# Performance work log

Measured on AMD Instinct MI355X. Metric: run time of the kernel, lower is better.

## Reference

```python
import jax, jax.numpy as jnp
import numpy as np

N_NODES = 50000
N_EDGES = 800000


def _spmm(edge_row, edge_col, edge_w, h):
    # sparse adj @ h via gather + segment-sum: adj[r,c] = edge_w
    msgs = edge_w[:, None] * h[edge_col]          # [E, D] gather
    return jax.ops.segment_sum(msgs, edge_row, num_segments=N_NODES)


def setup_inputs() -> dict:
    key = jax.random.key(0)
    ks = jax.random.split(key, 8)
    x = jax.random.normal(ks[0], (N_NODES, 256), dtype=jnp.float32)
    edge_row = jax.random.randint(ks[1], (N_EDGES,), 0, N_NODES, dtype=jnp.int32)
    edge_col = jax.random.randint(ks[2], (N_EDGES,), 0, N_NODES, dtype=jnp.int32)
    edge_w = jax.random.uniform(ks[3], (N_EDGES,), dtype=jnp.float32)
    W1 = jax.random.normal(ks[4], (256, 128), dtype=jnp.float32) * 0.06
    b1 = jnp.zeros((128,), dtype=jnp.float32)
    W2 = jax.random.normal(ks[5], (128, 32), dtype=jnp.float32) * 0.09
    b2 = jnp.zeros((32,), dtype=jnp.float32)
    return {"x": x, "edge_row": edge_row, "edge_col": edge_col,
            "edge_w": edge_w, "W1": W1, "b1": b1, "W2": W2, "b2": b2}


def reference(x, edge_row, edge_col, edge_w, W1, b1, W2, b2):
    # Layer 1: support = X @ W1 ; out = relu(A @ support + b1)
    # (dropout is identity in eval mode)
    h = jax.nn.relu(_spmm(edge_row, edge_col, edge_w, x @ W1) + b1)
    # Layer 2
    out = jax.nn.relu(_spmm(edge_row, edge_col, edge_w, h @ W2) + b2)
    return out
```

## Files before the change

### kernel.cpp

```cpp
#include <hip/hip_runtime.h>

#define N_NODES 50000
#define N_EDGES 800000
#define D0 256
#define D1 128
#define D2 32
#define CAP 64
#define SCAT_BLOCKS 391
#define G1_BLOCKS 782

typedef unsigned short u16;
typedef unsigned int   u32;
typedef __attribute__((ext_vector_type(8))) short bf16x8;
typedef __attribute__((ext_vector_type(4))) float f32x4;

__device__ inline u32 bf16rne(float f) {
    union { float f; u32 u; } c; c.f = f;
    return (c.u + 0x7FFFu + ((c.u >> 16) & 1u)) >> 16;
}
__device__ inline float bfhi(u32 v) {
    union { u32 u; float f; } c; c.u = v & 0xFFFF0000u; return c.f;
}
__device__ inline float bflo(u32 v) {
    union { u32 u; float f; } c; c.u = v << 16; return c.f;
}

__global__ __launch_bounds__(256) void front_kernel(const float* __restrict__ W1,
                                                    u16* __restrict__ Bsw1,
                                                    const float* __restrict__ W2,
                                                    u16* __restrict__ Bsw2) {
    const int bid = blockIdx.x;
    if (bid < 16) {
        const int id = bid * 256 + threadIdx.x;
        const int lane = id & 63;
        const int t    = (id >> 6) & 7;
        const int ks   = id >> 9;
        const int n     = t * 16 + (lane & 15);
        const int kbase = ks * 32 + (lane >> 4) * 8;
        u32 v[8];
        #pragma unroll
        for (int j = 0; j < 8; ++j) v[j] = bf16rne(W1[(kbase + j) * D1 + n]);
        uint4 w;
        w.x = v[0] | (v[1] << 16);
        w.y = v[2] | (v[3] << 16);
        w.z = v[4] | (v[5] << 16);
        w.w = v[6] | (v[7] << 16);
        ((uint4*)Bsw1)[id] = w;
    } else {
        const int id = (bid - 16) * 256 + threadIdx.x;
        const int lane = id & 63;
        const int t    = (id >> 6) & 1;
        const int ks   = id >> 7;
        const int n     = t * 16 + (lane & 15);
        const int kbase = ks * 32 + (lane >> 4) * 8;
        u32 v[8];
        #pragma unroll
        for (int j = 0; j < 8; ++j) v[j] = bf16rne(W2[(kbase + j) * D2 + n]);
        uint4 w;
        w.x = v[0] | (v[1] << 16);
        w.y = v[2] | (v[3] << 16);
        w.z = v[4] | (v[5] << 16);
        w.w = v[6] | (v[7] << 16);
        ((uint4*)Bsw2)[id] = w;
    }
}

__global__ __launch_bounds__(256) void mid_kernel(const float* __restrict__ x,
                                                  const u16* __restrict__ Bsw1,
                                                  u16* __restrict__ s1b,
                                                  const int* __restrict__ erow,
                                                  const int* __restrict__ ecol,
                                                  const float* __restrict__ ew,
                                                  int* __restrict__ cnt,
                                                  u32* __restrict__ eg) {
    const int bid = blockIdx.x;
    if (bid < G1_BLOCKS) {
        const int lane = threadIdx.x & 63;
        const int wave = threadIdx.x >> 6;
        const int rowbase = bid * 64 + wave * 16;
        const int m    = lane & 15;
        const int quad = lane >> 4;
        int arow = rowbase + m;
        if (arow >= N_NODES) arow = N_NODES - 1;
        const float* aptr = x + (size_t)arow * D0 + quad * 8;

        f32x4 acc[8];
        #pragma unroll
        for (int t = 0; t < 8; ++t) acc[t] = (f32x4){0.f, 0.f, 0.f, 0.f};

        #pragma unroll
        for (int ks = 0; ks < 8; ++ks) {
            const float4 f0 = *(const float4*)(aptr + ks * 32);
            const float4 f1 = *(const float4*)(aptr + ks * 32 + 4);
            bf16x8 a;
            a[0] = (short)bf16rne(f0.x); a[1] = (short)bf16rne(f0.y);
            a[2] = (short)bf16rne(f0.z); a[3] = (short)bf16rne(f0.w);
            a[4] = (short)bf16rne(f1.x); a[5] = (short)bf16rne(f1.y);
            a[6] = (short)bf16rne(f1.z); a[7] = (short)bf16rne(f1.w);
            const u16* bp = Bsw1 + ((size_t)(ks * 8) * 64 + lane) * 8;
            #pragma unroll
            for (int t = 0; t < 8; ++t) {
                const bf16x8 b = *(const bf16x8*)(bp + (size_t)t * 64 * 8);
                acc[t] = __builtin_amdgcn_mfma_f32_16x16x32_bf16(a, b, acc[t], 0, 0, 0);
            }
        }
        const int orow = rowbase + quad * 4;
        #pragma unroll
        for (int r = 0; r < 4; ++r) {
            const int row = orow + r;
            if (row < N_NODES) {
                u16* op = s1b + (size_t)row * D1 + m;
                #pragma unroll
                for (int t = 0; t < 8; ++t) op[t * 16] = (u16)bf16rne(acc[t][r]);
            }
        }
    } else {
        const int base = (bid - G1_BLOCKS) * 2048 + threadIdx.x;
        int  rows[8], cols[8];
        float ws[8];
        bool valid[8];
        #pragma unroll
        for (int k = 0; k < 8; ++k) {
            const int e = base + k * 256;
            valid[k] = e < N_EDGES;
            if (valid[k]) { rows[k] = erow[e]; cols[k] = ecol[e]; ws[k] = ew[e]; }
        }
        #pragma unroll
        for (int k = 0; k < 8; ++k) {
            if (valid[k]) {
                const int p = atomicAdd(&cnt[rows[k]], 1);
                if (p < CAP)
                    eg[(size_t)rows[k] * CAP + p] = (u32)cols[k] | (bf16rne(ws[k]) << 16);
            }
        }
    }
}

__global__ __launch_bounds__(256) void spmm_csr128_kernel(const int* __restrict__ cnt,
                                                          const u32* __restrict__ eg,
                                                          const u16* __restrict__ src,
                                                          const float* __restrict__ bias,
                                                          u16* __restrict__ dst) {
    const int lane = threadIdx.x;
    const int row  = blockIdx.x * 8 + threadIdx.y;
    if (row >= N_NODES) return;
    int len = cnt[row];
    if (len > CAP) len = CAP;
    const u32* ep = eg + (size_t)row * CAP;
    float4 a0 = {0.f,0.f,0.f,0.f}, a1 = {0.f,0.f,0.f,0.f};
    float4 a2 = {0.f,0.f,0.f,0.f}, a3 = {0.f,0.f,0.f,0.f};
    int j = 0;
    for (; j + 3 < len; j += 4) {
        const uint4 e4 = *(const uint4*)(ep + j);
        const uint2 v0 = ((const uint2*)(src + (size_t)(e4.x & 0xFFFFu) * D1))[lane];
        const uint2 v1 = ((const uint2*)(src + (size_t)(e4.y & 0xFFFFu) * D1))[lane];
        const uint2 v2 = ((const uint2*)(src + (size_t)(e4.z & 0xFFFFu) * D1))[lane];
        const uint2 v3 = ((const uint2*)(src + (size_t)(e4.w & 0xFFFFu) * D1))[lane];
        const float w0 = bfhi(e4.x), w1 = bfhi(e4.y), w2 = bfhi(e4.z), w3 = bfhi(e4.w);
        a0.x += w0 * bflo(v0.x); a0.y += w0 * bfhi(v0.x);
        a0.z += w0 * bflo(v0.y); a0.w += w0 * bfhi(v0.y);
        a1.x += w1 * bflo(v1.x); a1.y += w1 * bfhi(v1.x);
        a1.z += w1 * bflo(v1.y); a1.w += w1 * bfhi(v1.y);
        a2.x += w2 * bflo(v2.x); a2.y += w2 * bfhi(v2.x);
        a2.z += w2 * bflo(v2.y); a2.w += w2 * bfhi(v2.y);
        a3.x += w3 * bflo(v3.x); a3.y += w3 * bfhi(v3.x);
        a3.z += w3 * bflo(v3.y); a3.w += w3 * bfhi(v3.y);
    }
    for (; j < len; ++j) {
        const u32 e0 = ep[j];
        const float w0 = bfhi(e0);
        const uint2 v0 = ((const uint2*)(src + (size_t)(e0 & 0xFFFFu) * D1))[lane];
        a0.x += w0 * bflo(v0.x); a0.y += w0 * bfhi(v0.x);
        a0.z += w0 * bflo(v0.y); a0.w += w0 * bfhi(v0.y);
    }
    const float4 b4 = ((const float4*)bias)[lane];
    float rx = a0.x + a1.x + a2.x + a3.x + b4.x; rx = rx > 0.f ? rx : 0.f;
    float ry = a0.y + a1.y + a2.y + a3.y + b4.y; ry = ry > 0.f ? ry : 0.f;
    float rz = a0.z + a1.z + a2.z + a3.z + b4.z; rz = rz > 0.f ? rz : 0.f;
    float rw = a0.w + a1.w + a2.w + a3.w + b4.w; rw = rw > 0.f ? rw : 0.f;
    uint2 o;
    o.x = bf16rne(rx) | (bf16rne(ry) << 16);
    o.y = bf16rne(rz) | (bf16rne(rw) << 16);
    ((uint2*)(dst + (size_t)row * D1))[lane] = o;
}

__global__ __launch_bounds__(256) void gemm2_mfma_kernel(const u16* __restrict__ hb,
                                                         const u16* __restrict__ Bsw2,
                                                         u16* __restrict__ s2b) {
    const int lane = threadIdx.x & 63;
    const int wave = threadIdx.x >> 6;
    const int rowbase = blockIdx.x * 64 + wave * 16;
    const int m    = lane & 15;
    const int quad = lane >> 4;
    int arow = rowbase + m;
    if (arow >= N_NODES) arow = N_NODES - 1;
    const u16* aptr = hb + (size_t)arow * D1 + quad * 8;

    f32x4 acc0 = (f32x4){0.f,0.f,0.f,0.f};
    f32x4 acc1 = (f32x4){0.f,0.f,0.f,0.f};

    #pragma unroll
    for (int ks = 0; ks < 4; ++ks) {
        const bf16x8 a = *(const bf16x8*)(aptr + ks * 32);
        const u16* bp = Bsw2 + ((size_t)(ks * 2) * 64 + lane) * 8;
        const bf16x8 b0 = *(const bf16x8*)(bp);
        const bf16x8 b1 = *(const bf16x8*)(bp + (size_t)64 * 8);
        acc0 = __builtin_amdgcn_mfma_f32_16x16x32_bf16(a, b0, acc0, 0, 0, 0);
        acc1 = __builtin_amdgcn_mfma_f32_16x16x32_bf16(a, b1, acc1, 0, 0, 0);
    }
    const int orow = rowbase + quad * 4;
    #pragma unroll
    for (int r = 0; r < 4; ++r) {
        const int row = orow + r;
        if (row < N_NODES) {
            u16* op = s2b + (size_t)row * D2 + m;
            op[0]  = (u16)bf16rne(acc0[r]);
            op[16] = (u16)bf16rne(acc1[r]);
        }
    }
}

__global__ __launch_bounds__(256) void spmm_csr32_kernel(const int* __restrict__ cnt,
                                                         const u32* __restrict__ eg,
                                                         const u16* __restrict__ src,
                                                         const float* __restrict__ bias,
                                                         float* __restrict__ out) {
    const int lane = threadIdx.x;
    const int row  = blockIdx.x * 16 + threadIdx.y;
    if (row >= N_NODES) return;
    int len = cnt[row];
    if (len > CAP) len = CAP;
    const u32* ep = eg + (size_t)row * CAP;
    float ax0=0.f, ay0=0.f, ax1=0.f, ay1=0.f, ax2=0.f, ay2=0.f, ax3=0.f, ay3=0.f;
    int j = 0;
    for (; j + 3 < len; j += 4) {
        const uint4 e4 = *(const uint4*)(ep + j);
        const u32 v0 = ((const u32*)(src + (size_t)(e4.x & 0xFFFFu) * D2))[lane];
        const u32 v1 = ((const u32*)(src + (size_t)(e4.y & 0xFFFFu) * D2))[lane];
        const u32 v2 = ((const u32*)(src + (size_t)(e4.z & 0xFFFFu) * D2))[lane];
        const u32 v3 = ((const u32*)(src + (size_t)(e4.w & 0xFFFFu) * D2))[lane];
        const float w0 = bfhi(e4.x), w1 = bfhi(e4.y), w2 = bfhi(e4.z), w3 = bfhi(e4.w);
        ax0 += w0 * bflo(v0); ay0 += w0 * bfhi(v0);
        ax1 += w1 * bflo(v1); ay1 += w1 * bfhi(v1);
        ax2 += w2 * bflo(v2); ay2 += w2 * bfhi(v2);
        ax3 += w3 * bflo(v3); ay3 += w3 * bfhi(v3);
    }
    for (; j < len; ++j) {
        const u32 e0 = ep[j];
        const u32 v0 = ((const u32*)(src + (size_t)(e0 & 0xFFFFu) * D2))[lane];
        const float w0 = bfhi(e0);
        ax0 += w0 * bflo(v0); ay0 += w0 * bfhi(v0);
    }
    const float2 b2v = ((const float2*)bias)[lane];
    float vx = ax0 + ax1 + ax2 + ax3 + b2v.x; vx = vx > 0.f ? vx : 0.f;
    float vy = ay0 + ay1 + ay2 + ay3 + b2v.y; vy = vy > 0.f ? vy : 0.f;
    ((float2*)(out + (size_t)row * D2))[lane] = make_float2(vx, vy);
}

extern "C" void kernel_launch(void* const* d_in, const int* in_sizes, int n_in,
                              void* d_out, int out_size, void* d_ws, size_t ws_size,
                              hipStream_t stream) {
    const float* x    = (const float*)d_in[0];
    const int*   erow = (const int*)  d_in[1];
    const int*   ecol = (const int*)  d_in[2];
    const float* ew   = (const float*)d_in[3];
    const float* W1   = (const float*)d_in[4];
    const float* b1   = (const float*)d_in[5];
    const float* W2   = (const float*)d_in[6];
    const float* b2   = (const float*)d_in[7];
    float* out = (float*)d_out;

    int* cnt   = (int*)d_ws;
    u32* eg    = (u32*)(cnt + N_NODES);
    u16* Bsw1  = (u16*)(eg + (size_t)N_NODES * CAP);
    u16* Bsw2  = Bsw1 + 8 * 8 * 64 * 8;
    u16* s1b   = Bsw2 + 4 * 2 * 64 * 8;
    u16* hb    = s1b + (size_t)N_NODES * D1;
    u16* s2b   = hb + (size_t)N_NODES * D1;

    hipMemsetAsync(cnt, 0, N_NODES * sizeof(int), stream);
    front_kernel<<<18, 256, 0, stream>>>(W1, Bsw1, W2, Bsw2);
    mid_kernel<<<G1_BLOCKS + SCAT_BLOCKS, 256, 0, stream>>>(
        x, Bsw1, s1b, erow, ecol, ew, cnt, eg);
    spmm_csr128_kernel<<<(N_NODES + 7) / 8, dim3(32, 8), 0, stream>>>(cnt, eg, s1b, b1, hb);
    gemm2_mfma_kernel<<<(N_NODES + 63) / 64, 256, 0, stream>>>(hb, Bsw2, s2b);
    spmm_csr32_kernel<<<(N_NODES + 15) / 16, dim3(16, 16), 0, stream>>>(cnt, eg, s2b, b2, out);
}
```

Baseline: 214.8 us.

## Partition edge scatter by destination-row group and schedule it before GEMM1

The edge scatter now runs as 8 passes over the edge list. Each block handles one of 8 row ranges and only atomically appends edges whose destination row falls in that range, so atomics and eg writes land in a smaller, more cache-local region. Scatter blocks are also placed ahead of the GEMM1 blocks in the fused launch so they start first. The cost is reading erow 8 times over and launching more blocks.

Result: slower. 220.7 us (+2.8%).

```diff
diff --git a/kernel.cpp b/kernel.cpp
--- a/kernel.cpp
+++ b/kernel.cpp
@@ -6,6 +6,7 @@
 #define D1 128
 #define D2 32
 #define CAP 64
+#define ROWS_PER_GRP 6250
 #define SCAT_BLOCKS 391
 #define G1_BLOCKS 782
 
@@ -74,10 +75,32 @@
                                                   int* __restrict__ cnt,
                                                   u32* __restrict__ eg) {
     const int bid = blockIdx.x;
-    if (bid < G1_BLOCKS) {
+    if (bid < 8 * SCAT_BLOCKS) {
+        const int gsel  = bid & 7;
+        const int chunk = bid >> 3;
+        const int base  = chunk * 2048 + threadIdx.x;
+        int pos[8], rr[8], ee[8];
+        bool kp[8];
+        #pragma unroll
+        for (int k = 0; k < 8; ++k) {
+            const int e = base + k * 256;
+            int r = 0; bool keep = false;
+            if (e < N_EDGES) { r = erow[e]; keep = ((u32)r / ROWS_PER_GRP) == (u32)gsel; }
+            int p = -1;
+            if (keep) p = atomicAdd(&cnt[r], 1);
+            pos[k] = p; rr[k] = r; ee[k] = e; kp[k] = keep;
+        }
+        #pragma unroll
+        for (int k = 0; k < 8; ++k) {
+            if (kp[k] && pos[k] < CAP)
+                eg[(size_t)rr[k] * CAP + pos[k]] =
+                    (u32)ecol[ee[k]] | (bf16rne(ew[ee[k]]) << 16);
+        }
+    } else {
+        const int gb   = bid - 8 * SCAT_BLOCKS;
         const int lane = threadIdx.x & 63;
         const int wave = threadIdx.x >> 6;
-        const int rowbase = bid * 64 + wave * 16;
+        const int rowbase = gb * 64 + wave * 16;
         const int m    = lane & 15;
         const int quad = lane >> 4;
         int arow = rowbase + m;
@@ -112,25 +135,6 @@
                 u16* op = s1b + (size_t)row * D1 + m;
                 #pragma unroll
                 for (int t = 0; t < 8; ++t) op[t * 16] = (u16)bf16rne(acc[t][r]);
-            }
-        }
-    } else {
-        const int base = (bid - G1_BLOCKS) * 2048 + threadIdx.x;
-        int  rows[8], cols[8];
-        float ws[8];
-        bool valid[8];
-        #pragma unroll
-        for (int k = 0; k < 8; ++k) {
-            const int e = base + k * 256;
-            valid[k] = e < N_EDGES;
-            if (valid[k]) { rows[k] = erow[e]; cols[k] = ecol[e]; ws[k] = ew[e]; }
-        }
-        #pragma unroll
-        for (int k = 0; k < 8; ++k) {
-            if (valid[k]) {
-                const int p = atomicAdd(&cnt[rows[k]], 1);
-                if (p < CAP)
-                    eg[(size_t)rows[k] * CAP + p] = (u32)cols[k] | (bf16rne(ws[k]) << 16);
             }
         }
     }
@@ -280,7 +284,7 @@
 
     hipMemsetAsync(cnt, 0, N_NODES * sizeof(int), stream);
     front_kernel<<<18, 256, 0, stream>>>(W1, Bsw1, W2, Bsw2);
-    mid_kernel<<<G1_BLOCKS + SCAT_BLOCKS, 256, 0, stream>>>(
+    mid_kernel<<<8 * SCAT_BLOCKS + G1_BLOCKS, 256, 0, stream>>>(
         x, Bsw1, s1b, erow, ecol, ew, cnt, eg);
     spmm_csr128_kernel<<<(N_NODES + 7) / 8, dim3(32, 8), 0, stream>>>(cnt, eg, s1b, b1, hb);
     gemm2_mfma_kernel<<<(N_NODES + 63) / 64, 256, 0, stream>>>(hb, Bsw2, s2b);
```

## Split layer-1 SpMM into four 32-column passes and fold count reset into front kernel

Applied to the files above, without the earlier changes.

The layer-1 SpMM now runs as four column passes of 32 features each. Each of 16 lanes gathers 4 bytes instead of 32 lanes gathering 8 bytes, with 16 rows per block, so each pass's working set of the source matrix is smaller and more likely to stay in cache. The memset of the per-row counters becomes extra blocks in the front kernel, removing one launch. CAP drops from 64 to 48, shrinking the edge bucket array, but rows with more than 48 in-edges would now lose edges; with an average degree of 16 this is rare but possible. The edge list is also re-read four times.

Measured after the change: 218.3 us. About the same (+1.7%).

```diff
diff --git a/kernel.cpp b/kernel.cpp
--- a/kernel.cpp
+++ b/kernel.cpp
@@ -5,9 +5,10 @@
 #define D0 256
 #define D1 128
 #define D2 32
-#define CAP 64
+#define CAP 48
 #define SCAT_BLOCKS 391
 #define G1_BLOCKS 782
+#define SPMM1_RB 3125
 
 typedef unsigned short u16;
 typedef unsigned int   u32;
@@ -28,7 +29,8 @@
 __global__ __launch_bounds__(256) void front_kernel(const float* __restrict__ W1,
                                                     u16* __restrict__ Bsw1,
                                                     const float* __restrict__ W2,
-                                                    u16* __restrict__ Bsw2) {
+                                                    u16* __restrict__ Bsw2,
+                                                    int* __restrict__ cnt) {
     const int bid = blockIdx.x;
     if (bid < 16) {
         const int id = bid * 256 + threadIdx.x;
@@ -46,7 +48,7 @@
         w.z = v[4] | (v[5] << 16);
         w.w = v[6] | (v[7] << 16);
         ((uint4*)Bsw1)[id] = w;
-    } else {
+    } else if (bid < 18) {
         const int id = (bid - 16) * 256 + threadIdx.x;
         const int lane = id & 63;
         const int t    = (id >> 6) & 1;
@@ -62,6 +64,13 @@
         w.z = v[4] | (v[5] << 16);
         w.w = v[6] | (v[7] << 16);
         ((uint4*)Bsw2)[id] = w;
+    } else {
+        const int base = (bid - 18) * 2048 + threadIdx.x * 8;
+        #pragma unroll
+        for (int k = 0; k < 8; ++k) {
+            const int i = base + k;
+            if (i < N_NODES) cnt[i] = 0;
+        }
     }
 }
 
@@ -136,52 +145,43 @@
     }
 }
 
-__global__ __launch_bounds__(256) void spmm_csr128_kernel(const int* __restrict__ cnt,
-                                                          const u32* __restrict__ eg,
-                                                          const u16* __restrict__ src,
-                                                          const float* __restrict__ bias,
-                                                          u16* __restrict__ dst) {
+__global__ __launch_bounds__(256) void spmm1_kernel(const int* __restrict__ cnt,
+                                                    const u32* __restrict__ eg,
+                                                    const u16* __restrict__ src,
+                                                    const float* __restrict__ bias,
+                                                    u16* __restrict__ dst) {
+    const int pass = blockIdx.x / SPMM1_RB;
+    const int rb   = blockIdx.x % SPMM1_RB;
     const int lane = threadIdx.x;
-    const int row  = blockIdx.x * 8 + threadIdx.y;
-    if (row >= N_NODES) return;
+    const int row  = rb * 16 + threadIdx.y;
     int len = cnt[row];
     if (len > CAP) len = CAP;
     const u32* ep = eg + (size_t)row * CAP;
-    float4 a0 = {0.f,0.f,0.f,0.f}, a1 = {0.f,0.f,0.f,0.f};
-    float4 a2 = {0.f,0.f,0.f,0.f}, a3 = {0.f,0.f,0.f,0.f};
+    const u16* sq = src + pass * 32;
+    float ax0=0.f, ay0=0.f, ax1=0.f, ay1=0.f, ax2=0.f, ay2=0.f, ax3=0.f, ay3=0.f;
     int j = 0;
     for (; j + 3 < len; j += 4) {
         const uint4 e4 = *(const uint4*)(ep + j);
-        const uint2 v0 = ((const uint2*)(src + (size_t)(e4.x & 0xFFFFu) * D1))[lane];
-        const uint2 v1 = ((const uint2*)(src + (size_t)(e4.y & 0xFFFFu) * D1))[lane];
-        const uint2 v2 = ((const uint2*)(src + (size_t)(e4.z & 0xFFFFu) * D1))[lane];
-        const uint2 v3 = ((const uint2*)(src + (size_t)(e4.w & 0xFFFFu) * D1))[lane];
+        const u32 v0 = ((const u32*)(sq + (size_t)(e4.x & 0xFFFFu) * D1))[lane];
+        const u32 v1 = ((const u32*)(sq + (size_t)(e4.y & 0xFFFFu) * D1))[lane];
+        const u32 v2 = ((const u32*)(sq + (size_t)(e4.z & 0xFFFFu) * D1))[lane];
+        const u32 v3 = ((const u32*)(sq + (size_t)(e4.w & 0xFFFFu) * D1))[lane];
         const float w0 = bfhi(e4.x), w1 = bfhi(e4.y), w2 = bfhi(e4.z), w3 = bfhi(e4.w);
-        a0.x += w0 * bflo(v0.x); a0.y += w0 * bfhi(v0.x);
-        a0.z += w0 * bflo(v0.y); a0.w += w0 * bfhi(v0.y);
-        a1.x += w1 * bflo(v1.x); a1.y += w1 * bfhi(v1.x);
-        a1.z += w1 * bflo(v1.y); a1.w += w1 * bfhi(v1.y);
-        a2.x += w2 * bflo(v2.x); a2.y += w2 * bfhi(v2.x);
-        a2.z += w2 * bflo(v2.y); a2.w += w2 * bfhi(v2.y);
-        a3.x += w3 * bflo(v3.x); a3.y += w3 * bfhi(v3.x);
-        a3.z += w3 * bflo(v3.y); a3.w += w3 * bfhi(v3.y);
+        ax0 += w0 * bflo(v0); ay0 += w0 * bfhi(v0);
+        ax1 += w1 * bflo(v1); ay1 += w1 * bfhi(v1);
+        ax2 += w2 * bflo(v2); ay2 += w2 * bfhi(v2);
+        ax3 += w3 * bflo(v3); ay3 += w3 * bfhi(v3);
     }
     for (; j < len; ++j) {
         const u32 e0 = ep[j];
+        const u32 v0 = ((const u32*)(sq + (size_t)(e0 & 0xFFFFu) * D1))[lane];
         const float w0 = bfhi(e0);
-        const uint2 v0 = ((const uint2*)(src + (size_t)(e0 & 0xFFFFu) * D1))[lane];
-        a0.x += w0 * bflo(v0.x); a0.y += w0 * bfhi(v0.x);
-        a0.z += w0 * bflo(v0.y); a0.w += w0 * bfhi(v0.y);
-    }
-    const float4 b4 = ((const float4*)bias)[lane];
-    float rx = a0.x + a1.x + a2.x + a3.x + b4.x; rx = rx > 0.f ? rx : 0.f;
-    float ry = a0.y + a1.y + a2.y + a3.y + b4.y; ry = ry > 0.f ? ry : 0.f;
-    float rz = a0.z + a1.z + a2.z + a3.z + b4.z; rz = rz > 0.f ? rz : 0.f;
-    float rw = a0.w + a1.w + a2.w + a3.w + b4.w; rw = rw > 0.f ? rw : 0.f;
-    uint2 o;
-    o.x = bf16rne(rx) | (bf16rne(ry) << 16);
-    o.y = bf16rne(rz) | (bf16rne(rw) << 16);
-    ((uint2*)(dst + (size_t)row * D1))[lane] = o;
+        ax0 += w0 * bflo(v0); ay0 += w0 * bfhi(v0);
+    }
+    const float2 bv = ((const float2*)(bias + pass * 32))[lane];
+    float vx = ax0 + ax1 + ax2 + ax3 + bv.x; vx = vx > 0.f ? vx : 0.f;
+    float vy = ay0 + ay1 + ay2 + ay3 + bv.y; vy = vy > 0.f ? vy : 0.f;
+    ((u32*)(dst + (size_t)row * D1 + pass * 32))[lane] = bf16rne(vx) | (bf16rne(vy) << 16);
 }
 
 __global__ __launch_bounds__(256) void gemm2_mfma_kernel(const u16* __restrict__ hb,
@@ -278,11 +278,10 @@
     u16* hb    = s1b + (size_t)N_NODES * D1;
     u16* s2b   = hb + (size_t)N_NODES * D1;
 
-    hipMemsetAsync(cnt, 0, N_NODES * sizeof(int), stream);
-    front_kernel<<<18, 256, 0, stream>>>(W1, Bsw1, W2, Bsw2);
+    front_kernel<<<43, 256, 0, stream>>>(W1, Bsw1, W2, Bsw2, cnt);
     mid_kernel<<<G1_BLOCKS + SCAT_BLOCKS, 256, 0, stream>>>(
         x, Bsw1, s1b, erow, ecol, ew, cnt, eg);
-    spmm_csr128_kernel<<<(N_NODES + 7) / 8, dim3(32, 8), 0, stream>>>(cnt, eg, s1b, b1, hb);
+    spmm1_kernel<<<4 * SPMM1_RB, dim3(16, 16), 0, stream>>>(cnt, eg, s1b, b1, hb);
     gemm2_mfma_kernel<<<(N_NODES + 63) / 64, 256, 0, stream>>>(hb, Bsw2, s2b);
     spmm_csr32_kernel<<<(N_NODES + 15) / 16, dim3(16, 16), 0, stream>>>(cnt, eg, s2b, b2, out);
 }
```
